# Kernel optimization log

Measured on AMD Instinct MI355X. Metric: run time of the kernel, lower is better.

## Reference

```python
import jax, jax.numpy as jnp
import numpy as np

B, T, D, H = 4, 2048, 1024, 16
DK = D // H
LN_EPS = 1e-5


def setup_inputs() -> dict:
    key = jax.random.key(0)
    ks = jax.random.split(key, 12)
    s = 1.0 / np.sqrt(D)
    inp = {
        'x': jax.random.normal(ks[0], (B, T, D), jnp.float32),
        'Wq': jax.random.normal(ks[1], (D, D), jnp.float32) * s,
        'bq': jnp.zeros((D,), jnp.float32),
        'Wk': jax.random.normal(ks[2], (D, D), jnp.float32) * s,
        'bk': jnp.zeros((D,), jnp.float32),
        'Wv': jax.random.normal(ks[3], (D, D), jnp.float32) * s,
        'bv': jnp.zeros((D,), jnp.float32),
        'Wo': jax.random.normal(ks[4], (D, D), jnp.float32) * s,
        'bo': jnp.zeros((D,), jnp.float32),
        'ln_g': jnp.ones((D,), jnp.float32),
        'ln_b': jnp.zeros((D,), jnp.float32),
    }
    return inp


def reference(x, Wq, bq, Wk, bk, Wv, bv, Wo, bo, ln_g, ln_b):
    b, t, d = x.shape
    scale = jnp.sqrt(jnp.asarray(DK, x.dtype))
    # QKV projections -> [b, h, t, dk]
    q = (x @ Wq + bq).reshape(b, t, H, DK).transpose(0, 2, 1, 3)
    k = (x @ Wk + bk).reshape(b, t, H, DK).transpose(0, 2, 1, 3)
    v = (x @ Wv + bv).reshape(b, t, H, DK).transpose(0, 2, 1, 3)
    scores = jnp.einsum('bhqd,bhkd->bhqk', q, k) / scale  # [b,h,t,t]
    mask = jnp.tril(jnp.ones((t, t), x.dtype))[None, None]  # [1,1,t,t]
    neg = jnp.finfo(x.dtype).min
    scores = jnp.where(mask == 0, neg, scores)
    attn = jax.nn.softmax(scores, axis=-1)
    # mask-renormalize (as in the torch module)
    attn = attn * mask
    denom = attn.sum(-1, keepdims=True)
    attn = jnp.where(denom > 0, attn / denom, jnp.zeros_like(attn))
    ctx = jnp.einsum('bhqk,bhkd->bhqd', attn, v)  # [b,h,t,dk]
    ctx = ctx.transpose(0, 2, 1, 3).reshape(b, t, d)
    out = ctx @ Wo + bo
    y = out + x  # residual
    mu = y.mean(-1, keepdims=True)
    var = ((y - mu) ** 2).mean(-1, keepdims=True)
    return (y - mu) / jnp.sqrt(var + LN_EPS) * ln_g + ln_b
```

## Files before the change

### kernel.cpp

```cpp
#include <hip/hip_runtime.h>


using u16 = unsigned short;
using u32 = unsigned int;
typedef _Float16 f16x8 __attribute__((ext_vector_type(8)));
typedef float f32x4 __attribute__((ext_vector_type(4)));
typedef unsigned short u16x8 __attribute__((ext_vector_type(8)));

template <bool B> struct BoolTag { static constexpr bool v = B; };

__device__ inline u16 f2h_bits(float f) {
    _Float16 h = (_Float16)f;
    return __builtin_bit_cast(u16, h);
}

__device__ __forceinline__ void gload16(const void* g, void* l) {
    __builtin_amdgcn_global_load_lds(
        (const __attribute__((address_space(1))) void*)g,
        (__attribute__((address_space(3))) void*)l, 16, 0, 0);
}

__global__ __launch_bounds__(256) void convert_x_kernel(const float* __restrict__ x,
                                                        u16* __restrict__ xb) {
    size_t i = ((size_t)blockIdx.x * 256 + threadIdx.x) * 8;
    float4 a = *(const float4*)(x + i);
    float4 b = *(const float4*)(x + i + 4);
    u16x8 o;
    o[0] = f2h_bits(a.x); o[1] = f2h_bits(a.y); o[2] = f2h_bits(a.z); o[3] = f2h_bits(a.w);
    o[4] = f2h_bits(b.x); o[5] = f2h_bits(b.y); o[6] = f2h_bits(b.z); o[7] = f2h_bits(b.w);
    *(u16x8*)(xb + i) = o;
}

__global__ __launch_bounds__(256) void convert_wt_kernel(const float* __restrict__ W,
                                                         u16* __restrict__ Wt) {
    __shared__ float ts[64][68];
    const int k0 = blockIdx.x * 64, n0 = blockIdx.y * 64;
    const int tid = threadIdx.x, rr = tid >> 3, c = tid & 7;
#pragma unroll
    for (int p = 0; p < 2; p++) {
        int k = p * 32 + rr;
        float4 u = *(const float4*)(W + (size_t)(k0 + k) * 1024 + n0 + c * 8);
        float4 w = *(const float4*)(W + (size_t)(k0 + k) * 1024 + n0 + c * 8 + 4);
        *(float4*)&ts[k][c * 8] = u;
        *(float4*)&ts[k][c * 8 + 4] = w;
    }
    __syncthreads();
#pragma unroll
    for (int p = 0; p < 2; p++) {
        int n = p * 32 + rr;
        u16 o[8];
#pragma unroll
        for (int j = 0; j < 8; j++) o[j] = f2h_bits(ts[c * 8 + j][n]);
        *(u16x8*)(Wt + (size_t)(n0 + n) * 1024 + k0 + c * 8) = *(u16x8*)o;
    }
}

template <int MODE>
__global__ __launch_bounds__(512) void gemm256_kernel(
    const u16* __restrict__ A, const u16* __restrict__ Wt,
    const float* __restrict__ b0, const float* __restrict__ b1,
    const float* __restrict__ b2, u16* __restrict__ qo, u16* __restrict__ ko,
    u16* __restrict__ vo, float* __restrict__ outf,
    const float* __restrict__ xres) {
    constexpr int NBY = (MODE == 0) ? 12 : 4;
    __shared__ u16 As[3][128 * 64];
    __shared__ u16 Bs[3][256 * 64];

    const int bid = blockIdx.x;
    const int cpx = (MODE == 0) ? 96 : 32;
    const int swz = (bid & 7) * cpx + (bid >> 3);
    const int bx = swz / NBY, by = swz % NBY;
    const size_t row0 = (size_t)bx * 128;
    const size_t col0 = (size_t)by * 256;

    const int tid = threadIdx.x, lane = tid & 63;
    const int wid = tid >> 6, wm = wid >> 2, wn = wid & 3;
    const int l15 = lane & 15, lg = lane >> 4;
    const int rr = tid >> 3, c8 = tid & 7;
    const int scw = (c8 ^ (rr & 7)) * 8;

    f32x4 acc[4][4] = {};

    auto stage_half = [&](int kt, int p, int h) {
        const int k0 = kt * 64;
        if (h == 0) {
            gload16(A + (row0 + rr) * 1024 + k0 + scw, As[p] + tid * 8);
            gload16(Wt + (col0 + rr) * 1024 + k0 + scw, Bs[p] + tid * 8);
            gload16(Wt + (col0 + 64 + rr) * 1024 + k0 + scw,
                    Bs[p] + (512 + tid) * 8);
        } else {
            gload16(A + (row0 + 64 + rr) * 1024 + k0 + scw,
                    As[p] + (512 + tid) * 8);
            gload16(Wt + (col0 + 128 + rr) * 1024 + k0 + scw,
                    Bs[p] + (1024 + tid) * 8);
            gload16(Wt + (col0 + 192 + rr) * 1024 + k0 + scw,
                    Bs[p] + (1536 + tid) * 8);
        }
    };

    stage_half(0, 0, 0); stage_half(0, 0, 1);
    stage_half(1, 1, 0); stage_half(1, 1, 1);
    asm volatile("s_waitcnt vmcnt(6)" ::: "memory");
    __builtin_amdgcn_s_barrier();

    int p = 0, pn = 1, pp = 2;
    for (int t = 0; t < 16; t++) {
        const bool st = (t + 2 < 16);
        const u16* Ab = As[p];
        const u16* Bb = Bs[p];
#pragma unroll
        for (int kc = 0; kc < 2; kc++) {
            if (st) stage_half(t + 2, pp, kc);
            f16x8 af[4], bf[4];
#pragma unroll
            for (int n = 0; n < 4; n++) {
                int rb = wn * 64 + n * 16 + l15;
                bf[n] = *(const f16x8*)(Bb + rb * 64 + ((kc * 4 + lg) ^ (rb & 7)) * 8);
            }
#pragma unroll
            for (int m = 0; m < 4; m++) {
                int ra = wm * 64 + m * 16 + l15;
                af[m] = *(const f16x8*)(Ab + ra * 64 + ((kc * 4 + lg) ^ (ra & 7)) * 8);
            }
            __builtin_amdgcn_sched_barrier(0);
            if (kc == 1) {
                if (st) asm volatile("s_waitcnt vmcnt(6)" ::: "memory");
                else    asm volatile("s_waitcnt vmcnt(0)" ::: "memory");
                __builtin_amdgcn_sched_barrier(0);
            }
            __builtin_amdgcn_s_barrier();
            __builtin_amdgcn_sched_barrier(0);
            __builtin_amdgcn_s_setprio(1);
#pragma unroll
            for (int m = 0; m < 4; m++)
#pragma unroll
                for (int n = 0; n < 4; n++)
                    acc[m][n] = __builtin_amdgcn_mfma_f32_16x16x32_f16(
                        af[m], bf[n], acc[m][n], 0, 0, 0);
            __builtin_amdgcn_s_setprio(0);
            __builtin_amdgcn_sched_barrier(0);
            __builtin_amdgcn_s_barrier();
        }
        int tmp = p; p = pn; pn = pp; pp = tmp;
    }

    if (MODE == 0) {
        const int zsel = by >> 2;
        u16* ob = zsel == 0 ? qo : (zsel == 1 ? ko : vo);
        const float* bias = zsel == 0 ? b0 : (zsel == 1 ? b1 : b2);
        const float qs = zsel == 0 ? 0.18033688f : 1.0f;
#pragma unroll
        for (int m = 0; m < 4; m++) {
#pragma unroll
            for (int n = 0; n < 4; n++) {
                size_t col = col0 + wn * 64 + n * 16 + l15;
                size_t colz = col & 1023;
                float bb = bias[colz];
#pragma unroll
                for (int r = 0; r < 4; r++) {
                    size_t row = row0 + wm * 64 + m * 16 + lg * 4 + r;
                    ob[row * 1024 + colz] = f2h_bits((acc[m][n][r] + bb) * qs);
                }
            }
        }
    } else {
#pragma unroll
        for (int m = 0; m < 4; m++) {
#pragma unroll
            for (int n = 0; n < 4; n++) {
                size_t col = col0 + wn * 64 + n * 16 + l15;
                float bb = b0[col];
#pragma unroll
                for (int r = 0; r < 4; r++) {
                    size_t row = row0 + wm * 64 + m * 16 + lg * 4 + r;
                    size_t idx = row * 1024 + col;
                    outf[idx] = acc[m][n][r] + bb + xres[idx];
                }
            }
        }
    }
}

__global__ __launch_bounds__(256) void transpose_v_kernel(const u16* __restrict__ V,
                                                          u16* __restrict__ Vt) {
    __shared__ u16 ts[64][72];
    const int bh = blockIdx.y;
    const int b = bh >> 4, h = bh & 15;
    const int t0 = blockIdx.x * 64;
    const int tid = threadIdx.x, rr = tid >> 3, c = tid & 7;
#pragma unroll
    for (int p = 0; p < 2; p++) {
        int t = p * 32 + rr;
        *(u16x8*)&ts[t][c * 8] =
            *(const u16x8*)(V + ((size_t)b * 2048 + t0 + t) * 1024 + h * 64 + c * 8);
    }
    __syncthreads();
#pragma unroll
    for (int p = 0; p < 2; p++) {
        int d = p * 32 + rr;
        u16 o[8];
#pragma unroll
        for (int j = 0; j < 8; j++) o[j] = ts[c * 8 + j][d];
        *(u16x8*)(Vt + ((size_t)bh * 64 + d) * 2048 + t0 + c * 8) = *(u16x8*)o;
    }
}

__global__ __launch_bounds__(256) void attn_kernel(const u16* __restrict__ Q,
                                                   const u16* __restrict__ Kb,
                                                   const u16* __restrict__ Vt,
                                                   u16* __restrict__ ctx) {
    __shared__ u16 Ks[2][64 * 64];
    __shared__ u16 Vs[2][64 * 64];
    __shared__ u16 Ps[8][16 * 64];

    const int bh = blockIdx.x;
    const int b = bh >> 4, h = bh & 15;
    const int qb = 15 - (int)blockIdx.y;
    const int tid = threadIdx.x, lane = tid & 63, wid = tid >> 6;
    const int l15 = lane & 15, lg = lane >> 4;
    const int q0w = qb * 128 + wid * 32;
    const int send = qb * 128;

    const int rr = tid >> 3, c8 = tid & 7;
    const int scw = (c8 ^ (rr & 7)) * 8;
    const size_t kbase = ((size_t)b * 2048) * 1024 + h * 64 + scw;
    const size_t vbase = ((size_t)bh * 64 + rr) * 2048 + scw;

    f16x8 qv[2][2];
#pragma unroll
    for (int qf = 0; qf < 2; qf++) {
        size_t qoff = ((size_t)b * 2048 + q0w + qf * 16 + l15) * 1024 + h * 64 + lg * 8;
        qv[qf][0] = *(const f16x8*)(Q + qoff);
        qv[qf][1] = *(const f16x8*)(Q + qoff + 32);
    }

    const int swk0 = (lg ^ (l15 & 7)) * 8;
    const int swk1 = ((4 + lg) ^ (l15 & 7)) * 8;
    u16* Pw0 = Ps[wid * 2 + 0] + l15 * 64;
    u16* Pw1 = Ps[wid * 2 + 1] + l15 * 64;

    f32x4 acc[2][4] = {};
    float psum[2] = {0.0f, 0.0f};

    auto stage = [&](int s, int bf) {
#pragma unroll
        for (int ph = 0; ph < 2; ph++) {
            gload16(Kb + kbase + (size_t)(s + ph * 32 + rr) * 1024,
                    Ks[bf] + (ph * 256 + wid * 64) * 8);
            gload16(Vt + vbase + (size_t)(ph * 32) * 2048 + s,
                    Vs[bf] + (ph * 256 + wid * 64) * 8);
        }
    };

    auto body = [&](int s, int bf, auto maskc) {
        constexpr bool MASK = decltype(maskc)::v;
        f32x4 sc[2][4];
#pragma unroll
        for (int c = 0; c < 4; c++) {
            const u16* kp = Ks[bf] + (c * 16 + l15) * 64;
            f16x8 kf0 = *(const f16x8*)(kp + swk0);
            f16x8 kf1 = *(const f16x8*)(kp + swk1);
#pragma unroll
            for (int qf = 0; qf < 2; qf++) {
                f32x4 z = {};
                z = __builtin_amdgcn_mfma_f32_16x16x32_f16(kf0, qv[qf][0], z, 0, 0, 0);
                z = __builtin_amdgcn_mfma_f32_16x16x32_f16(kf1, qv[qf][1], z, 0, 0, 0);
                sc[qf][c] = z;
            }
        }
#pragma unroll
        for (int qf = 0; qf < 2; qf++) {
            u16* Pw = qf ? Pw1 : Pw0;
#pragma unroll
            for (int c = 0; c < 4; c++) {
                float pv[4];
#pragma unroll
                for (int r = 0; r < 4; r++) {
                    float e = __builtin_amdgcn_exp2f(fminf(sc[qf][c][r], 15.0f));
                    if (MASK) {
                        int kk = s + c * 16 + lg * 4 + r;
                        e = (kk <= q0w + qf * 16 + l15) ? e : 0.0f;
                    }
                    psum[qf] += e;
                    pv[r] = e;
                }
                uint2 w;
                w.x = __builtin_bit_cast(u32, __builtin_amdgcn_cvt_pkrtz(pv[0], pv[1]));
                w.y = __builtin_bit_cast(u32, __builtin_amdgcn_cvt_pkrtz(pv[2], pv[3]));
                int gsw = (((c * 2 + (lg >> 1)) ^ (l15 & 7)) << 3) + (lg & 1) * 4;
                *(uint2*)(Pw + gsw) = w;
            }
        }
        f16x8 pa0[2], pa1[2];
#pragma unroll
        for (int qf = 0; qf < 2; qf++) {
            const u16* Pw = qf ? Pw1 : Pw0;
            pa0[qf] = *(const f16x8*)(Pw + ((lg ^ (l15 & 7)) << 3));
            pa1[qf] = *(const f16x8*)(Pw + (((4 + lg) ^ (l15 & 7)) << 3));
        }
#pragma unroll
        for (int dt = 0; dt < 4; dt++) {
            const u16* vp = Vs[bf] + (dt * 16 + l15) * 64;
            f16x8 vf0 = *(const f16x8*)(vp + swk0);
            f16x8 vf1 = *(const f16x8*)(vp + swk1);
#pragma unroll
            for (int qf = 0; qf < 2; qf++) {
                acc[qf][dt] =
                    __builtin_amdgcn_mfma_f32_16x16x32_f16(pa0[qf], vf0, acc[qf][dt], 0, 0, 0);
                acc[qf][dt] =
                    __builtin_amdgcn_mfma_f32_16x16x32_f16(pa1[qf], vf1, acc[qf][dt], 0, 0, 0);
            }
        }
    };

    stage(0, 0);
    int cur = 0;
    for (int s = 0; s < send; s += 64) {
        __syncthreads();
        stage(s + 64, cur ^ 1);
        body(s, cur, BoolTag<false>{});
        cur ^= 1;
    }
    __syncthreads();
    stage(send + 64, cur ^ 1);
    body(send, cur, BoolTag<true>{});
    cur ^= 1;
    __syncthreads();
    if (wid >= 2) body(send + 64, cur, BoolTag<true>{});

#pragma unroll
    for (int qf = 0; qf < 2; qf++) {
        psum[qf] += __shfl_xor(psum[qf], 16);
        psum[qf] += __shfl_xor(psum[qf], 32);
    }
#pragma unroll
    for (int qf = 0; qf < 2; qf++) {
        float inv = 1.0f / psum[qf];
#pragma unroll
        for (int r = 0; r < 4; r++) {
            float ir = __shfl(inv, lg * 4 + r);
            size_t row = (size_t)b * 2048 + q0w + qf * 16 + lg * 4 + r;
#pragma unroll
            for (int dt = 0; dt < 4; dt++)
                ctx[row * 1024 + h * 64 + dt * 16 + l15] = f2h_bits(acc[qf][dt][r] * ir);
        }
    }
}

__global__ __launch_bounds__(256) void ln_kernel(const float* __restrict__ y,
                                                 const float* __restrict__ g,
                                                 const float* __restrict__ bb,
                                                 float* __restrict__ out) {
    const int r = blockIdx.x, tid = threadIdx.x;
    float4 v = *(const float4*)(y + (size_t)r * 1024 + tid * 4);
    float s = v.x + v.y + v.z + v.w;
    float sq = v.x * v.x + v.y * v.y + v.z * v.z + v.w * v.w;
#pragma unroll
    for (int ofs = 1; ofs < 64; ofs <<= 1) {
        s += __shfl_xor(s, ofs);
        sq += __shfl_xor(sq, ofs);
    }
    __shared__ float as[4], aq[4];
    if ((tid & 63) == 0) { as[tid >> 6] = s; aq[tid >> 6] = sq; }
    __syncthreads();
    s = as[0] + as[1] + as[2] + as[3];
    sq = aq[0] + aq[1] + aq[2] + aq[3];
    float mu = s * (1.0f / 1024.0f);
    float var = sq * (1.0f / 1024.0f) - mu * mu;
    float rstd = rsqrtf(var + 1e-5f);
    float4 gv = *(const float4*)(g + tid * 4);
    float4 bv = *(const float4*)(bb + tid * 4);
    float4 o4;
    o4.x = (v.x - mu) * rstd * gv.x + bv.x;
    o4.y = (v.y - mu) * rstd * gv.y + bv.y;
    o4.z = (v.z - mu) * rstd * gv.z + bv.z;
    o4.w = (v.w - mu) * rstd * gv.w + bv.w;
    *(float4*)(out + (size_t)r * 1024 + tid * 4) = o4;
}

extern "C" void kernel_launch(void* const* d_in, const int* in_sizes, int n_in,
                              void* d_out, int out_size, void* d_ws, size_t ws_size,
                              hipStream_t stream) {
    const float* x  = (const float*)d_in[0];
    const float* Wq = (const float*)d_in[1];
    const float* bq = (const float*)d_in[2];
    const float* Wk = (const float*)d_in[3];
    const float* bk = (const float*)d_in[4];
    const float* Wv = (const float*)d_in[5];
    const float* bv = (const float*)d_in[6];
    const float* Wo = (const float*)d_in[7];
    const float* bo = (const float*)d_in[8];
    const float* lg = (const float*)d_in[9];
    const float* lb = (const float*)d_in[10];
    float* out = (float*)d_out;

    char* ws = (char*)d_ws;
    u16* xb = (u16*)(ws + 0);
    u16* wt = (u16*)(ws + 16777216);
    u16* q  = (u16*)(ws + 25165824);
    u16* k  = (u16*)(ws + 41943040);
    u16* v  = (u16*)(ws + 58720256);
    u16* vt = (u16*)(ws + 75497472);
    u16* cx = (u16*)(ws + 92274688);
    float* y = (float*)(ws + 109051904);

    convert_x_kernel<<<4096, 256, 0, stream>>>(x, xb);
    dim3 gw(16, 16);
    convert_wt_kernel<<<gw, 256, 0, stream>>>(Wq, wt);
    convert_wt_kernel<<<gw, 256, 0, stream>>>(Wk, wt + 1048576);
    convert_wt_kernel<<<gw, 256, 0, stream>>>(Wv, wt + 2097152);
    convert_wt_kernel<<<gw, 256, 0, stream>>>(Wo, wt + 3145728);

    gemm256_kernel<0><<<768, 512, 0, stream>>>(xb, wt, bq, bk, bv, q, k, v,
                                               nullptr, nullptr);
    transpose_v_kernel<<<dim3(32, 64), 256, 0, stream>>>(v, vt);
    attn_kernel<<<dim3(64, 16), 256, 0, stream>>>(q, k, vt, cx);
    gemm256_kernel<1><<<256, 512, 0, stream>>>(cx, wt + 3145728, bo, nullptr,
                                               nullptr, nullptr, nullptr, nullptr,
                                               y, x);
    ln_kernel<<<8192, 256, 0, stream>>>(y, lg, lb, out);
}
```

Baseline: 202.5 us.

## Software-pipeline LDS fragment loads against MFMA in GEMM main loop

Restructures the GEMM K-loop so that the LDS fragment reads for the next half-tile are issued before the MFMAs on the current half-tile, using double-buffered register fragments. The number of barriers per iteration drops, and the stage buffers rotate through pointers instead of indices. The aim is to hide LDS read latency and barrier stalls behind matrix-core work. The cost is higher register pressure from holding two fragment sets, and a more delicate vmcnt and barrier ordering.

```diff
diff --git a/kernel.cpp b/kernel.cpp
--- a/kernel.cpp
+++ b/kernel.cpp
@@ -80,68 +80,78 @@
     const int scw = (c8 ^ (rr & 7)) * 8;
 
     f32x4 acc[4][4] = {};
-
-    auto stage_half = [&](int kt, int p, int h) {
+    f16x8 Aa[4], Ba[4], Ab[4], Bb[4];
+
+    auto stage_half = [&](int kt, u16* dA, u16* dB, int h) {
         const int k0 = kt * 64;
         if (h == 0) {
-            gload16(A + (row0 + rr) * 1024 + k0 + scw, As[p] + tid * 8);
-            gload16(Wt + (col0 + rr) * 1024 + k0 + scw, Bs[p] + tid * 8);
-            gload16(Wt + (col0 + 64 + rr) * 1024 + k0 + scw,
-                    Bs[p] + (512 + tid) * 8);
+            gload16(A + (row0 + rr) * 1024 + k0 + scw, dA + tid * 8);
+            gload16(Wt + (col0 + rr) * 1024 + k0 + scw, dB + tid * 8);
+            gload16(Wt + (col0 + 64 + rr) * 1024 + k0 + scw, dB + (512 + tid) * 8);
         } else {
-            gload16(A + (row0 + 64 + rr) * 1024 + k0 + scw,
-                    As[p] + (512 + tid) * 8);
-            gload16(Wt + (col0 + 128 + rr) * 1024 + k0 + scw,
-                    Bs[p] + (1024 + tid) * 8);
-            gload16(Wt + (col0 + 192 + rr) * 1024 + k0 + scw,
-                    Bs[p] + (1536 + tid) * 8);
+            gload16(A + (row0 + 64 + rr) * 1024 + k0 + scw, dA + (512 + tid) * 8);
+            gload16(Wt + (col0 + 128 + rr) * 1024 + k0 + scw, dB + (1024 + tid) * 8);
+            gload16(Wt + (col0 + 192 + rr) * 1024 + k0 + scw, dB + (1536 + tid) * 8);
         }
     };
 
-    stage_half(0, 0, 0); stage_half(0, 0, 1);
-    stage_half(1, 1, 0); stage_half(1, 1, 1);
+    auto ldops = [&](const u16* bA, const u16* bB, int kcv, f16x8* Af, f16x8* Bf) {
+        const int swo = ((kcv * 4 + lg) ^ (l15 & 7)) * 8;
+#pragma unroll
+        for (int n = 0; n < 4; n++)
+            Bf[n] = *(const f16x8*)(bB + (wn * 64 + n * 16 + l15) * 64 + swo);
+#pragma unroll
+        for (int m = 0; m < 4; m++)
+            Af[m] = *(const f16x8*)(bA + (wm * 64 + m * 16 + l15) * 64 + swo);
+    };
+
+    auto domfma = [&](const f16x8* Af, const f16x8* Bf) {
+        __builtin_amdgcn_s_setprio(1);
+#pragma unroll
+        for (int m = 0; m < 4; m++)
+#pragma unroll
+            for (int n = 0; n < 4; n++)
+                acc[m][n] = __builtin_amdgcn_mfma_f32_16x16x32_f16(
+                    Af[m], Bf[n], acc[m][n], 0, 0, 0);
+        __builtin_amdgcn_s_setprio(0);
+    };
+
+    u16 *pA = &As[0][0], *pnA = &As[1][0], *ppA = &As[2][0];
+    u16 *pB = &Bs[0][0], *pnB = &Bs[1][0], *ppB = &Bs[2][0];
+
+    stage_half(0, pA, pB, 0);
+    stage_half(0, pA, pB, 1);
+    stage_half(1, pnA, pnB, 0);
+    stage_half(1, pnA, pnB, 1);
     asm volatile("s_waitcnt vmcnt(6)" ::: "memory");
+    __builtin_amdgcn_sched_barrier(0);
     __builtin_amdgcn_s_barrier();
-
-    int p = 0, pn = 1, pp = 2;
+    ldops(pA, pB, 0, Aa, Ba);
+
+#pragma unroll 1
     for (int t = 0; t < 16; t++) {
-        const bool st = (t + 2 < 16);
-        const u16* Ab = As[p];
-        const u16* Bb = Bs[p];
-#pragma unroll
-        for (int kc = 0; kc < 2; kc++) {
-            if (st) stage_half(t + 2, pp, kc);
-            f16x8 af[4], bf[4];
-#pragma unroll
-            for (int n = 0; n < 4; n++) {
-                int rb = wn * 64 + n * 16 + l15;
-                bf[n] = *(const f16x8*)(Bb + rb * 64 + ((kc * 4 + lg) ^ (rb & 7)) * 8);
-            }
-#pragma unroll
-            for (int m = 0; m < 4; m++) {
-                int ra = wm * 64 + m * 16 + l15;
-                af[m] = *(const f16x8*)(Ab + ra * 64 + ((kc * 4 + lg) ^ (ra & 7)) * 8);
-            }
-            __builtin_amdgcn_sched_barrier(0);
-            if (kc == 1) {
-                if (st) asm volatile("s_waitcnt vmcnt(6)" ::: "memory");
-                else    asm volatile("s_waitcnt vmcnt(0)" ::: "memory");
-                __builtin_amdgcn_sched_barrier(0);
-            }
-            __builtin_amdgcn_s_barrier();
-            __builtin_amdgcn_sched_barrier(0);
-            __builtin_amdgcn_s_setprio(1);
-#pragma unroll
-            for (int m = 0; m < 4; m++)
-#pragma unroll
-                for (int n = 0; n < 4; n++)
-                    acc[m][n] = __builtin_amdgcn_mfma_f32_16x16x32_f16(
-                        af[m], bf[n], acc[m][n], 0, 0, 0);
-            __builtin_amdgcn_s_setprio(0);
+        ldops(pA, pB, 1, Ab, Bb);
+        if (t < 14) stage_half(t + 2, ppA, ppB, 0);
+        __builtin_amdgcn_sched_barrier(0);
+        domfma(Aa, Ba);
+        __builtin_amdgcn_sched_barrier(0);
+        if (t < 15) {
+            if (t < 14) asm volatile("s_waitcnt vmcnt(3)" ::: "memory");
+            else        asm volatile("s_waitcnt vmcnt(0)" ::: "memory");
             __builtin_amdgcn_sched_barrier(0);
             __builtin_amdgcn_s_barrier();
-        }
-        int tmp = p; p = pn; pn = pp; pp = tmp;
+            ldops(pnA, pnB, 0, Aa, Ba);
+            if (t < 14) stage_half(t + 2, ppA, ppB, 1);
+        }
+        __builtin_amdgcn_sched_barrier(0);
+        domfma(Ab, Bb);
+        __builtin_amdgcn_sched_barrier(0);
+        if (t < 15) {
+            __builtin_amdgcn_s_barrier();
+            u16* tp;
+            tp = pA; pA = pnA; pnA = ppA; ppA = tp;
+            tp = pB; pB = pnB; pnB = ppB; ppB = tp;
+        }
     }
 
     if (MODE == 0) {
```

New measurement: 197.0 us. -2.7%, faster.
